# Optimization experiments

Measured on AMD Instinct MI355X. Metric: run time of the kernel, lower is better.

The kernel has to match this reference:

```python
import jax, jax.numpy as jnp
import numpy as np

HID, OUT, EMB, NL = 256, 128, 1024, 4
NR, NP_, NM = 16384, 40000, 30000
E = 200000
NTYPES = 3  # lin_nodes keys: protein, molecule, reaction


def setup_inputs() -> dict:
    key = jax.random.key(0)
    ks = jax.random.split(key, 32)
    f32 = jnp.float32
    inp = {}
    inp["x_reaction"] = jax.random.normal(ks[0], (NR, EMB), f32)
    inp["x_protein"] = jax.random.normal(ks[1], (NP_, EMB), f32)
    inp["x_molecule"] = jax.random.normal(ks[2], (NM, EMB), f32)
    inp["ei_p2r_src"] = jax.random.randint(ks[3], (E,), 0, NP_, jnp.int32)
    inp["ei_p2r_dst"] = jax.random.randint(ks[4], (E,), 0, NR, jnp.int32)
    inp["ei_m2r_src"] = jax.random.randint(ks[5], (E,), 0, NM, jnp.int32)
    inp["ei_m2r_dst"] = jax.random.randint(ks[6], (E,), 0, NR, jnp.int32)
    inp["ei_r2p_src"] = jax.random.randint(ks[7], (E,), 0, NR, jnp.int32)
    inp["ei_r2p_dst"] = jax.random.randint(ks[8], (E,), 0, NP_, jnp.int32)
    inp["ei_r2m_src"] = jax.random.randint(ks[9], (E,), 0, NR, jnp.int32)
    inp["ei_r2m_dst"] = jax.random.randint(ks[10], (E,), 0, NM, jnp.int32)
    inp["output_notes_opt"] = jax.random.normal(ks[11], (NR, EMB), f32)
    inp["output_types"] = jax.random.randint(ks[12], (NR,), 0, NTYPES, jnp.int32)
    s = 0.02
    # layer 0 SAGE params (lazy in_dim = EMB), one set per edge type (4 edge types)
    inp["Wl0"] = jax.random.normal(ks[13], (4, EMB, HID), f32) * s
    inp["Wr0"] = jax.random.normal(ks[14], (4, EMB, HID), f32) * s
    inp["bl0"] = jnp.zeros((4, HID), f32)
    # layers 1..3 SAGE params (in_dim = HID)
    inp["Wl"] = jax.random.normal(ks[15], (NL - 1, 4, HID, HID), f32) * s
    inp["Wr"] = jax.random.normal(ks[16], (NL - 1, 4, HID, HID), f32) * s
    inp["bl"] = jnp.zeros((NL - 1, 4, HID), f32)
    inp["W_reaction"] = jax.random.normal(ks[17], (HID, OUT), f32) * s
    inp["b_reaction"] = jnp.zeros((OUT,), f32)
    inp["W_nodes"] = jax.random.normal(ks[18], (NTYPES, EMB, OUT), f32) * s
    inp["b_nodes"] = jnp.zeros((NTYPES, OUT), f32)
    return inp


def _sage(x_src, x_dst, src, dst, n_dst, Wl, bl, Wr):
    # PyG SAGEConv (aggr='mean'): lin_l(mean_{j->i} x_j) + lin_r(x_i); lin_l has bias.
    g = x_src[src]                                              # [E, d] gather
    s = jax.ops.segment_sum(g, dst, num_segments=n_dst)          # [n_dst, d]
    cnt = jax.ops.segment_sum(jnp.ones((src.shape[0],), x_src.dtype), dst, num_segments=n_dst)
    mean = s / jnp.maximum(cnt, 1.0)[:, None]
    return mean @ Wl + bl + x_dst @ Wr


def _hetero_layer(xr, xp, xm, edges, Wl, bl, Wr):
    # HeteroConv(aggr='sum'): sum SAGE outputs per destination node type.
    (ps, pd), (ms, md), (rps, rpd), (rms, rmd) = edges
    new_r = (_sage(xp, xr, ps, pd, NR, Wl[0], bl[0], Wr[0])
             + _sage(xm, xr, ms, md, NR, Wl[1], bl[1], Wr[1]))
    new_p = _sage(xr, xp, rps, rpd, NP_, Wl[2], bl[2], Wr[2])
    new_m = _sage(xr, xm, rms, rmd, NM, Wl[3], bl[3], Wr[3])
    return new_r, new_p, new_m


def reference(x_reaction, x_protein, x_molecule,
              ei_p2r_src, ei_p2r_dst, ei_m2r_src, ei_m2r_dst,
              ei_r2p_src, ei_r2p_dst, ei_r2m_src, ei_r2m_dst,
              output_notes_opt, output_types,
              Wl0, bl0, Wr0, Wl, bl, Wr,
              W_reaction, b_reaction, W_nodes, b_nodes):
    edges = ((ei_p2r_src, ei_p2r_dst), (ei_m2r_src, ei_m2r_dst),
             (ei_r2p_src, ei_r2p_dst), (ei_r2m_src, ei_r2m_dst))
    xr, xp, xm = _hetero_layer(x_reaction, x_protein, x_molecule, edges, Wl0, bl0, Wr0)
    for l in range(NL - 1):
        xr, xp, xm = _hetero_layer(xr, xp, xm, edges, Wl[l], bl[l], Wr[l])
    reaction_out = xr @ W_reaction + b_reaction                  # [NR, OUT]
    # lin_nodes[t](v) per output node: project with all type linears, select by type id
    projs = jnp.einsum('ke,ted->ktd', output_notes_opt, W_nodes) + b_nodes[None]  # [NR, T, OUT]
    node_out = jnp.take_along_axis(projs, output_types[:, None, None].astype(jnp.int32), axis=1)[:, 0, :]
    # cosine similarity along dim=1, torch-style eps clamp on the norm product
    num = jnp.sum(reaction_out * node_out, axis=-1)
    den = jnp.maximum(jnp.linalg.norm(reaction_out, axis=-1) * jnp.linalg.norm(node_out, axis=-1), 1e-8)
    return (num / den + 1.0) * 0.5
```

## Files before the change

kernel.cpp:

```cpp
#include <hip/hip_runtime.h>
#include <hip/hip_bf16.h>
#include <math.h>
#include <stdint.h>

#define NR_ 16384
#define NP2_ 40000
#define NM_ 30000
#define NE_ 200000
#define EMB_ 1024
#define HID_ 256
#define OUTD_ 128

typedef __attribute__((ext_vector_type(8))) short bf16x8;
typedef __attribute__((ext_vector_type(4))) float f32x4;
typedef __attribute__((ext_vector_type(8))) unsigned short us8;

__device__ __forceinline__ unsigned short f2bf(float f) {
    return __builtin_bit_cast(unsigned short, __float2bfloat16(f));
}
__device__ __forceinline__ float bf2f(unsigned short u) {
    uint32_t v = ((uint32_t)u) << 16;
    return __builtin_bit_cast(float, v);
}

struct Csr4 {
    const int* src[4]; const int* dst[4];
    int* offs[4]; int* cur[4]; int* csr[4];
    int n[4];
};
__global__ void k_zero4(Csr4 c) {
    int y = blockIdx.y;
    int i = blockIdx.x * 256 + threadIdx.x;
    if (i < c.n[y]) c.cur[y][i] = 0;
}
__global__ void k_deg4(Csr4 c) {
    int y = blockIdx.y;
    int i = blockIdx.x * 256 + threadIdx.x;
    if (i < NE_) atomicAdd(&c.cur[y][c.dst[y][i]], 1);
}
__global__ void k_scanA(Csr4 c, int* __restrict__ csum) {
    int y = blockIdx.y;
    int n = c.n[y];
    int ch = blockIdx.x;
    int nch = (n + 1023) >> 10;
    if (ch >= nch) return;
    const int* deg = c.cur[y];
    int* offs = c.offs[y];
    __shared__ int ts[256];
    int base = ch << 10;
    int t = threadIdx.x;
    int v[4];
    int s = 0;
    #pragma unroll
    for (int k = 0; k < 4; ++k) {
        int i = base + t * 4 + k;
        v[k] = (i < n) ? deg[i] : 0;
        s += v[k];
    }
    ts[t] = s;
    __syncthreads();
    for (int st = 1; st < 256; st <<= 1) {
        int x = ts[t];
        int xo = (t >= st) ? ts[t - st] : 0;
        __syncthreads();
        ts[t] = x + xo;
        __syncthreads();
    }
    int run = (t > 0) ? ts[t - 1] : 0;
    #pragma unroll
    for (int k = 0; k < 4; ++k) {
        int i = base + t * 4 + k;
        if (i < n) offs[i] = run;
        run += v[k];
    }
    if (t == 255) csum[y * 40 + ch] = ts[255];
}
__global__ void k_scanB(Csr4 c, int* __restrict__ csum) {
    int y = threadIdx.x;
    if (y < 4) {
        int n = c.n[y];
        int nch = (n + 1023) >> 10;
        int acc = 0;
        for (int i = 0; i < nch; ++i) {
            int v = csum[y * 40 + i];
            csum[y * 40 + i] = acc;
            acc += v;
        }
        c.offs[y][n] = acc;
    }
}
__global__ void k_scanC(Csr4 c, const int* __restrict__ csum) {
    int y = blockIdx.y;
    int i = blockIdx.x * 256 + threadIdx.x;
    if (i < c.n[y]) {
        int v = c.offs[y][i] + csum[y * 40 + (i >> 10)];
        c.offs[y][i] = v;
        c.cur[y][i] = v;
    }
}
__global__ void k_scatter4(Csr4 c) {
    int y = blockIdx.y;
    int i = blockIdx.x * 256 + threadIdx.x;
    if (i < NE_) {
        int d = c.dst[y][i];
        int p = atomicAdd(&c.cur[y][d], 1);
        c.csr[y][p] = c.src[y][i];
    }
}

struct WItem { const float* a; const float* b; unsigned short* dst; int k; int n; };
struct WBatch { WItem it[32]; };
__global__ void k_wconvT(WBatch wb) {
    WItem w = wb.it[blockIdx.y];
    int total = w.k * w.n;
    int kmask = w.k - 1;
    int shift = (w.k == 1024) ? 10 : 8;
    for (int idx = blockIdx.x * 256 + threadIdx.x; idx < total; idx += gridDim.x * 256) {
        int k = idx & kmask, n = idx >> shift;
        float v = w.a[(size_t)k * w.n + n];
        if (w.b) v += w.b[(size_t)k * w.n + n];
        w.dst[idx] = f2bf(v);
    }
}

struct GSeg {
    const void* A; const unsigned short* Bt; void* C; const float* bias;
    int lda, ldc, M, K, ntn, blk0;
};
struct GBatch { GSeg s[3]; int b1, b2, tot; };

template <bool OBF>
__global__ __launch_bounds__(256, 3) void k_gemmb(GBatch gb) {
    __shared__ __align__(16) unsigned short As[128 * 64];
    __shared__ __align__(16) unsigned short Bs[128 * 64];
    const int tid = threadIdx.x;
    const int lane = tid & 63;
    int nwg = gb.tot;
    int o = blockIdx.x;
    int q = nwg >> 3, r = nwg & 7;
    int xcd = o & 7, j = o >> 3;
    int wg = (xcd < r ? xcd * (q + 1) : r * (q + 1) + (xcd - r) * q) + j;
    const int si = (wg >= gb.b1) + (wg >= gb.b2);
    const GSeg sg = gb.s[si];
    const int local = wg - sg.blk0;
    const int bm = (local / sg.ntn) * 128;
    const int bn = (local % sg.ntn) * 128;
    const int lda = sg.lda, ldc = sg.ldc, M = sg.M, K = sg.K;
    const unsigned short* __restrict__ Bt = sg.Bt;
    const float* __restrict__ bias = sg.bias;

    const int wave = tid >> 6;
    const int wr = (wave >> 1) * 64;
    const int wc = (wave & 1) * 64;
    const int frow = lane & 15;
    const int fkc = lane >> 4;
    f32x4 acc[4][4] = {};

    for (int k0 = 0; k0 < K; k0 += 64) {
        #pragma unroll
        for (int i = 0; i < 4; ++i) {
            int c = tid + i * 256;
            int row = c >> 3, kc = c & 7;
            int srck = k0 + ((kc ^ (row & 7)) << 3);
            int ga = min(bm + row, M - 1);
            __builtin_amdgcn_global_load_lds(
                (const __attribute__((address_space(1))) unsigned int*)((const unsigned short*)sg.A + (size_t)ga * lda + srck),
                (__attribute__((address_space(3))) unsigned int*)(As + (size_t)c * 8), 16, 0, 0);
            __builtin_amdgcn_global_load_lds(
                (const __attribute__((address_space(1))) unsigned int*)(Bt + (size_t)(bn + row) * K + srck),
                (__attribute__((address_space(3))) unsigned int*)(Bs + (size_t)c * 8), 16, 0, 0);
        }
        __syncthreads();
        #pragma unroll
        for (int kk = 0; kk < 2; ++kk) {
            bf16x8 af[4], bfr[4];
            #pragma unroll
            for (int m = 0; m < 4; ++m) {
                int row = wr + m * 16 + frow;
                int kc = kk * 4 + fkc;
                af[m] = *(const bf16x8*)(As + (size_t)((row << 3) + (kc ^ (row & 7))) * 8);
            }
            #pragma unroll
            for (int n = 0; n < 4; ++n) {
                int row = wc + n * 16 + frow;
                int kc = kk * 4 + fkc;
                bfr[n] = *(const bf16x8*)(Bs + (size_t)((row << 3) + (kc ^ (row & 7))) * 8);
            }
            #pragma unroll
            for (int m = 0; m < 4; ++m)
                #pragma unroll
                for (int n = 0; n < 4; ++n)
                    acc[m][n] = __builtin_amdgcn_mfma_f32_16x16x32_bf16(bfr[n], af[m], acc[m][n], 0, 0, 0);
        }
        __syncthreads();
    }

    const int ccol0 = (lane >> 4) << 2;
    #pragma unroll
    for (int m = 0; m < 4; ++m) {
        int row = bm + wr + m * 16 + frow;
        if (row < M) {
            #pragma unroll
            for (int n = 0; n < 4; ++n) {
                int col = bn + wc + n * 16 + ccol0;
                f32x4 v = acc[m][n];
                if (bias) {
                    v[0] += bias[col + 0];
                    v[1] += bias[col + 1];
                    v[2] += bias[col + 2];
                    v[3] += bias[col + 3];
                }
                if constexpr (OBF) {
                    ushort4 oo;
                    oo.x = f2bf(v[0]); oo.y = f2bf(v[1]); oo.z = f2bf(v[2]); oo.w = f2bf(v[3]);
                    *(ushort4*)((unsigned short*)sg.C + (size_t)row * ldc + col) = oo;
                } else {
                    *(float4*)((float*)sg.C + (size_t)row * ldc + col) = make_float4(v[0], v[1], v[2], v[3]);
                }
            }
        }
    }
}

template <bool OBF>
__global__ __launch_bounds__(256, 3) void k_gemma(GBatch gb) {
    __shared__ __align__(16) unsigned short As[128 * 64];
    __shared__ __align__(16) unsigned short Bs[2][128 * 64];
    const int tid = threadIdx.x;
    const int lane = tid & 63;
    int nwg = gb.tot;
    int o = blockIdx.x;
    int q = nwg >> 3, r = nwg & 7;
    int xcd = o & 7, j = o >> 3;
    int wg = (xcd < r ? xcd * (q + 1) : r * (q + 1) + (xcd - r) * q) + j;
    const int si = (wg >= gb.b1) + (wg >= gb.b2);
    const GSeg sg = gb.s[si];
    const int local = wg - sg.blk0;
    const int bm = (local / sg.ntn) * 128;
    const int bn = (local % sg.ntn) * 128;
    const int lda = sg.lda, ldc = sg.ldc, M = sg.M, K = sg.K;
    const unsigned short* __restrict__ Bt = sg.Bt;
    const float* __restrict__ bias = sg.bias;

    const int wave = tid >> 6;
    const int wr = (wave >> 1) * 64;
    const int wc = (wave & 1) * 64;
    const int frow = lane & 15;
    const int fkc = lane >> 4;
    f32x4 acc[4][4] = {};
    float4 ra0[4], ra1[4];

#define ALOAD(kk0) do {                                                                    \
    _Pragma("unroll")                                                                      \
    for (int i = 0; i < 4; ++i) {                                                          \
        int c = tid + i * 256, rw = c >> 3, kc = c & 7;                                    \
        int srck = (kk0) + ((kc ^ (rw & 7)) << 3);                                         \
        int ga = min(bm + rw, M - 1);                                                      \
        const float* Af = (const float*)sg.A + (size_t)ga * lda + srck;                    \
        ra0[i] = *(const float4*)Af;                                                       \
        ra1[i] = *(const float4*)(Af + 4);                                                 \
    } } while (0)

#define AWRITE() do {                                                                      \
    _Pragma("unroll")                                                                      \
    for (int i = 0; i < 4; ++i) {                                                          \
        int c = tid + i * 256;                                                             \
        us8 oo;                                                                            \
        oo[0] = f2bf(ra0[i].x); oo[1] = f2bf(ra0[i].y);                                    \
        oo[2] = f2bf(ra0[i].z); oo[3] = f2bf(ra0[i].w);                                    \
        oo[4] = f2bf(ra1[i].x); oo[5] = f2bf(ra1[i].y);                                    \
        oo[6] = f2bf(ra1[i].z); oo[7] = f2bf(ra1[i].w);                                    \
        *(us8*)(As + (size_t)c * 8) = oo;                                                  \
    } } while (0)

#define STAGE_B(bufi, kk0) do {                                                            \
    _Pragma("unroll")                                                                      \
    for (int i = 0; i < 4; ++i) {                                                          \
        int c = tid + i * 256, rw = c >> 3, kc = c & 7;                                    \
        int srck = (kk0) + ((kc ^ (rw & 7)) << 3);                                         \
        __builtin_amdgcn_global_load_lds(                                                  \
            (const __attribute__((address_space(1))) unsigned int*)(Bt + (size_t)(bn + rw) * K + srck), \
            (__attribute__((address_space(3))) unsigned int*)(&Bs[bufi][(size_t)c * 8]), 16, 0, 0); \
    } } while (0)

#define COMPUTE(bufi) do {                                                                 \
    _Pragma("unroll")                                                                      \
    for (int kk = 0; kk < 2; ++kk) {                                                       \
        bf16x8 af[4], bfr[4];                                                              \
        _Pragma("unroll")                                                                  \
        for (int m = 0; m < 4; ++m) {                                                      \
            int rw = wr + m * 16 + frow;                                                   \
            int kc = kk * 4 + fkc;                                                         \
            af[m] = *(const bf16x8*)(As + (size_t)((rw << 3) + (kc ^ (rw & 7))) * 8);      \
        }                                                                                  \
        _Pragma("unroll")                                                                  \
        for (int n = 0; n < 4; ++n) {                                                      \
            int rw = wc + n * 16 + frow;                                                   \
            int kc = kk * 4 + fkc;                                                         \
            bfr[n] = *(const bf16x8*)(&Bs[bufi][(size_t)((rw << 3) + (kc ^ (rw & 7))) * 8]); \
        }                                                                                  \
        _Pragma("unroll")                                                                  \
        for (int m = 0; m < 4; ++m)                                                        \
            _Pragma("unroll")                                                              \
            for (int n = 0; n < 4; ++n)                                                    \
                acc[m][n] = __builtin_amdgcn_mfma_f32_16x16x32_bf16(bfr[n], af[m], acc[m][n], 0, 0, 0); \
    } } while (0)

    const int nt = K >> 6;
    ALOAD(0);
    STAGE_B(0, 0);
    AWRITE();
    asm volatile("s_waitcnt lgkmcnt(0)" ::: "memory");
    __builtin_amdgcn_sched_barrier(0);
    for (int t = 0; t < nt; ++t) {
        if (t + 1 < nt) {
            ALOAD((t + 1) << 6);
            STAGE_B((t + 1) & 1, (t + 1) << 6);
            asm volatile("s_waitcnt vmcnt(12)" ::: "memory");
        } else {
            asm volatile("s_waitcnt vmcnt(0)" ::: "memory");
        }
        __builtin_amdgcn_s_barrier();
        __builtin_amdgcn_sched_barrier(0);
        COMPUTE(t & 1);
        asm volatile("s_waitcnt lgkmcnt(0)" ::: "memory");
        __builtin_amdgcn_s_barrier();
        __builtin_amdgcn_sched_barrier(0);
        if (t + 1 < nt) {
            AWRITE();
            asm volatile("s_waitcnt lgkmcnt(0)" ::: "memory");
            __builtin_amdgcn_sched_barrier(0);
        }
    }
#undef ALOAD
#undef AWRITE
#undef STAGE_B
#undef COMPUTE

    const int ccol0 = (lane >> 4) << 2;
    #pragma unroll
    for (int m = 0; m < 4; ++m) {
        int row = bm + wr + m * 16 + frow;
        if (row < M) {
            #pragma unroll
            for (int n = 0; n < 4; ++n) {
                int col = bn + wc + n * 16 + ccol0;
                f32x4 v = acc[m][n];
                if (bias) {
                    v[0] += bias[col + 0];
                    v[1] += bias[col + 1];
                    v[2] += bias[col + 2];
                    v[3] += bias[col + 3];
                }
                if constexpr (OBF) {
                    ushort4 oo;
                    oo.x = f2bf(v[0]); oo.y = f2bf(v[1]); oo.z = f2bf(v[2]); oo.w = f2bf(v[3]);
                    *(ushort4*)((unsigned short*)sg.C + (size_t)row * ldc + col) = oo;
                } else {
                    *(float4*)((float*)sg.C + (size_t)row * ldc + col) = make_float4(v[0], v[1], v[2], v[3]);
                }
            }
        }
    }
}

struct ASeg {
    const int* offsA; const int* csrA; const unsigned short* projA; int ldpA; const float* biasA;
    const int* offsB; const int* csrB; const unsigned short* projB; int ldpB; const float* biasB;
    unsigned short* outx; int ldo; int ndst; int blk0;
};
struct ABatch { ASeg s[3]; int b1, b2; };

__device__ __forceinline__ void agg_sum16(const int* __restrict__ csr, int beg, int end,
                                          const unsigned short* __restrict__ base, int ldp,
                                          int lane, float* __restrict__ s) {
    int half = lane >> 5;
    for (int b = beg; b < end; b += 64) {
        int cnt = min(64, end - b);
        int myidx = csr[min(b + lane, end - 1)];
        int g = 0;
        for (; g + 3 < cnt; g += 4) {
            int i0 = __shfl(myidx, g + half);
            int i1 = __shfl(myidx, g + 2 + half);
            us8 u0 = *(const us8*)(base + (size_t)i0 * ldp);
            us8 u1 = *(const us8*)(base + (size_t)i1 * ldp);
            #pragma unroll
            for (int j = 0; j < 8; ++j) s[j] += bf2f(u0[j]) + bf2f(u1[j]);
        }
        for (; g + 1 < cnt; g += 2) {
            int i0 = __shfl(myidx, g + half);
            us8 u0 = *(const us8*)(base + (size_t)i0 * ldp);
            #pragma unroll
            for (int j = 0; j < 8; ++j) s[j] += bf2f(u0[j]);
        }
        if (g < cnt) {
            int i0 = __shfl(myidx, g);
            if (half == 0) {
                us8 u0 = *(const us8*)(base + (size_t)i0 * ldp);
                #pragma unroll
                for (int j = 0; j < 8; ++j) s[j] += bf2f(u0[j]);
            }
        }
    }
}

__global__ __launch_bounds__(256) void k_aggb(ABatch ab) {
    int b = blockIdx.x;
    int si = (b >= ab.b1) + (b >= ab.b2);
    const ASeg sg = ab.s[si];
    int node = (b - sg.blk0) * 4 + (threadIdx.x >> 6);
    int lane = threadIdx.x & 63;
    if (node >= sg.ndst) return;
    const int off = (lane & 31) * 8;

    float r[8];
    {
        float s[8] = {};
        int beg = sg.offsA[node], end = sg.offsA[node + 1];
        agg_sum16(sg.csrA, beg, end, sg.projA + off, sg.ldpA, lane, s);
        #pragma unroll
        for (int j = 0; j < 8; ++j) s[j] += __shfl_xor(s[j], 32);
        float inv = 1.f / fmaxf((float)(end - beg), 1.f);
        float4 b0 = *(const float4*)(sg.biasA + off);
        float4 b1 = *(const float4*)(sg.biasA + off + 4);
        r[0] = s[0] * inv + b0.x; r[1] = s[1] * inv + b0.y;
        r[2] = s[2] * inv + b0.z; r[3] = s[3] * inv + b0.w;
        r[4] = s[4] * inv + b1.x; r[5] = s[5] * inv + b1.y;
        r[6] = s[6] * inv + b1.z; r[7] = s[7] * inv + b1.w;
    }
    if (sg.csrB) {
        float s[8] = {};
        int beg = sg.offsB[node], end = sg.offsB[node + 1];
        agg_sum16(sg.csrB, beg, end, sg.projB + off, sg.ldpB, lane, s);
        #pragma unroll
        for (int j = 0; j < 8; ++j) s[j] += __shfl_xor(s[j], 32);
        float inv = 1.f / fmaxf((float)(end - beg), 1.f);
        float4 b0 = *(const float4*)(sg.biasB + off);
        float4 b1 = *(const float4*)(sg.biasB + off + 4);
        r[0] += s[0] * inv + b0.x; r[1] += s[1] * inv + b0.y;
        r[2] += s[2] * inv + b0.z; r[3] += s[3] * inv + b0.w;
        r[4] += s[4] * inv + b1.x; r[5] += s[5] * inv + b1.y;
        r[6] += s[6] * inv + b1.z; r[7] += s[7] * inv + b1.w;
    }

    if (lane < 32) {
        unsigned short* op = sg.outx + (size_t)node * sg.ldo + off;
        us8 cur = *(const us8*)op;
        us8 w;
        #pragma unroll
        for (int j = 0; j < 8; ++j) w[j] = f2bf(bf2f(cur[j]) + r[j]);
        *(us8*)op = w;
    }
}

__global__ __launch_bounds__(256) void k_cos(const float* __restrict__ ro,
                                             const float* __restrict__ pr,
                                             const int* __restrict__ types,
                                             float* __restrict__ out, int nr) {
    int row = blockIdx.x * 4 + (threadIdx.x >> 6);
    int lane = threadIdx.x & 63;
    if (row >= nr) return;
    int t = types[row];
    float2 r = ((const float2*)(ro + (size_t)row * OUTD_))[lane];
    float2 nn = ((const float2*)(pr + (size_t)row * 384 + t * OUTD_))[lane];
    float num = r.x * nn.x + r.y * nn.y;
    float d1 = r.x * r.x + r.y * r.y;
    float d2 = nn.x * nn.x + nn.y * nn.y;
    #pragma unroll
    for (int s = 1; s < 64; s <<= 1) {
        num += __shfl_xor(num, s);
        d1 += __shfl_xor(d1, s);
        d2 += __shfl_xor(d2, s);
    }
    if (lane == 0) out[row] = (num / fmaxf(sqrtf(d1) * sqrtf(d2), 1e-8f) + 1.f) * 0.5f;
}

extern "C" void kernel_launch(void* const* d_in, const int* in_sizes, int n_in,
                              void* d_out, int out_size, void* d_ws, size_t ws_size,
                              hipStream_t stream) {
    const float* x_r0 = (const float*)d_in[0];
    const float* x_p0 = (const float*)d_in[1];
    const float* x_m0 = (const float*)d_in[2];
    const int* e_src[4] = {(const int*)d_in[3], (const int*)d_in[5], (const int*)d_in[7], (const int*)d_in[9]};
    const int* e_dst[4] = {(const int*)d_in[4], (const int*)d_in[6], (const int*)d_in[8], (const int*)d_in[10]};
    const float* notes = (const float*)d_in[11];
    const int* types = (const int*)d_in[12];
    const float* Wl0 = (const float*)d_in[13];
    const float* Wr0 = (const float*)d_in[14];
    const float* bl0 = (const float*)d_in[15];
    const float* WlL = (const float*)d_in[16];
    const float* WrL = (const float*)d_in[17];
    const float* blL = (const float*)d_in[18];
    const float* Wre = (const float*)d_in[19];
    const float* bre = (const float*)d_in[20];
    const float* Wn  = (const float*)d_in[21];
    const float* bn  = (const float*)d_in[22];
    float* out = (float*)d_out;

    uintptr_t base = (uintptr_t)d_ws;
    auto alloc = [&](size_t bytes) -> void* {
        uintptr_t p = (base + 255) & ~(uintptr_t)255;
        base = p + bytes;
        return (void*)p;
    };
    unsigned short* Rb[2] = {(unsigned short*)alloc((size_t)NR_ * 768 * 2),
                             (unsigned short*)alloc((size_t)NR_ * 768 * 2)};
    unsigned short* Pb[2] = {(unsigned short*)alloc((size_t)NP2_ * 512 * 2),
                             (unsigned short*)alloc((size_t)NP2_ * 512 * 2)};
    unsigned short* Mb[2] = {(unsigned short*)alloc((size_t)NM_ * 512 * 2),
                             (unsigned short*)alloc((size_t)NM_ * 512 * 2)};
    float* ro = (float*)alloc((size_t)NR_ * OUTD_ * 4);
    float* pr = (float*)alloc((size_t)NR_ * 384 * 4);
    unsigned short* wbf = (unsigned short*)alloc((size_t)4000000 * 2);
    int* csum = (int*)alloc(160 * 4);
    int nd[4] = {NR_, NR_, NP2_, NM_};
    Csr4 cs{};
    for (int t = 0; t < 4; ++t) {
        cs.src[t] = e_src[t]; cs.dst[t] = e_dst[t]; cs.n[t] = nd[t];
        cs.offs[t] = (int*)alloc(((size_t)nd[t] + 1) * 4);
        cs.cur[t]  = (int*)alloc((size_t)nd[t] * 4);
        cs.csr[t]  = (int*)alloc((size_t)NE_ * 4);
    }

    unsigned short *BR[4], *BP[4], *BM[4], *Bre, *Bn;
    {
        WBatch wb{};
        int cnt = 0;
        size_t woff = 0;
        auto add = [&](const float* a, const float* bb, int K, int N) -> unsigned short* {
            unsigned short* dst = wbf + woff;
            woff += (size_t)K * N;
            wb.it[cnt] = WItem{a, bb, dst, K, N};
            ++cnt;
            return dst;
        };
        const size_t w0 = (size_t)EMB_ * HID_;
        const size_t wl = (size_t)HID_ * HID_;
        for (int l = 0; l < 4; ++l) {
            int K = (l == 0) ? EMB_ : HID_;
            const float* Wr_ = (l == 0) ? Wr0 : WrL + (size_t)(l - 1) * 4 * wl;
            const float* Wl_ = (l == 0) ? Wl0 : WlL + (size_t)(l - 1) * 4 * wl;
            size_t ws_ = (l == 0) ? w0 : wl;
            BR[l] = add(Wr_ + 0 * ws_, Wr_ + 1 * ws_, K, HID_);
            add(Wl_ + 2 * ws_, nullptr, K, HID_);
            add(Wl_ + 3 * ws_, nullptr, K, HID_);
            BP[l] = add(Wr_ + 2 * ws_, nullptr, K, HID_);
            add(Wl_ + 0 * ws_, nullptr, K, HID_);
            BM[l] = add(Wr_ + 3 * ws_, nullptr, K, HID_);
            add(Wl_ + 1 * ws_, nullptr, K, HID_);
        }
        Bre = add(Wre, nullptr, HID_, OUTD_);
        Bn = add(Wn + 0 * (size_t)EMB_ * OUTD_, nullptr, EMB_, OUTD_);
        add(Wn + 1 * (size_t)EMB_ * OUTD_, nullptr, EMB_, OUTD_);
        add(Wn + 2 * (size_t)EMB_ * OUTD_, nullptr, EMB_, OUTD_);
        k_wconvT<<<dim3(128, cnt), 256, 0, stream>>>(wb);
    }

    k_zero4<<<dim3((NP2_ + 255) / 256, 4), 256, 0, stream>>>(cs);
    k_deg4<<<dim3((NE_ + 255) / 256, 4), 256, 0, stream>>>(cs);
    k_scanA<<<dim3(40, 4), 256, 0, stream>>>(cs, csum);
    k_scanB<<<1, 64, 0, stream>>>(cs, csum);
    k_scanC<<<dim3((NP2_ + 255) / 256, 4), 256, 0, stream>>>(cs, csum);
    k_scatter4<<<dim3((NE_ + 255) / 256, 4), 256, 0, stream>>>(cs);

    const int MT_R = (NR_ + 127) / 128;
    const int MT_P = (NP2_ + 127) / 128;
    const int MT_M = (NM_ + 127) / 128;
    auto seg = [](const void* A, const unsigned short* Bt, void* C, const float* bias,
                  int lda, int ldc, int M, int K, int ntn, int blk0) -> GSeg {
        return GSeg{A, Bt, C, bias, lda, ldc, M, K, ntn, blk0};
    };

    const int AB_R = (NR_ + 3) / 4, AB_P = (NP2_ + 3) / 4, AB_M = (NM_ + 3) / 4;

    for (int l = 0; l < 4; ++l) {
        int K = (l == 0) ? EMB_ : HID_;
        unsigned short* R = Rb[l & 1];
        unsigned short* P = Pb[l & 1];
        unsigned short* M = Mb[l & 1];
        const float* bl_ = (l == 0) ? bl0 : blL + (size_t)(l - 1) * 4 * HID_;

        GBatch gb{};
        int nR = MT_R * 6, nP = MT_P * 4, nM = MT_M * 4;
        if (l == 0) {
            gb.s[0] = seg(x_r0, BR[0], R, nullptr, EMB_, 768, NR_, EMB_, 6, 0);
            gb.s[1] = seg(x_p0, BP[0], P, nullptr, EMB_, 512, NP2_, EMB_, 4, nR);
            gb.s[2] = seg(x_m0, BM[0], M, nullptr, EMB_, 512, NM_, EMB_, 4, nR + nP);
        } else {
            gb.s[0] = seg(Rb[(l - 1) & 1], BR[l], R, nullptr, 768, 768, NR_, K, 6, 0);
            gb.s[1] = seg(Pb[(l - 1) & 1], BP[l], P, nullptr, 512, 512, NP2_, K, 4, nR);
            gb.s[2] = seg(Mb[(l - 1) & 1], BM[l], M, nullptr, 512, 512, NM_, K, 4, nR + nP);
        }
        gb.b1 = nR; gb.b2 = nR + nP; gb.tot = nR + nP + nM;
        if (l == 0) k_gemma<true><<<gb.tot, 256, 0, stream>>>(gb);
        else        k_gemmb<true><<<gb.tot, 256, 0, stream>>>(gb);

        ABatch ab{};
        ab.s[0] = ASeg{cs.offs[0], cs.csr[0], P + 256, 512, bl_ + 0 * HID_,
                       cs.offs[1], cs.csr[1], M + 256, 512, bl_ + 1 * HID_,
                       R, 768, NR_, 0};
        ab.s[1] = ASeg{cs.offs[2], cs.csr[2], R + 256, 768, bl_ + 2 * HID_,
                       nullptr, nullptr, nullptr, 0, nullptr,
                       P, 512, NP2_, AB_R};
        ab.s[2] = ASeg{cs.offs[3], cs.csr[3], R + 512, 768, bl_ + 3 * HID_,
                       nullptr, nullptr, nullptr, 0, nullptr,
                       M, 512, NM_, AB_R + AB_P};
        ab.b1 = AB_R; ab.b2 = AB_R + AB_P;
        k_aggb<<<AB_R + AB_P + AB_M, 256, 0, stream>>>(ab);
    }

    {
        GBatch g1{};
        g1.s[0] = seg(Rb[1], Bre, ro, bre, 768, OUTD_, NR_, HID_, 1, 0);
        g1.b1 = g1.b2 = g1.tot = MT_R;
        k_gemmb<false><<<g1.tot, 256, 0, stream>>>(g1);
        GBatch g2{};
        g2.s[0] = seg(notes, Bn, pr, bn, EMB_, 384, NR_, EMB_, 3, 0);
        g2.b1 = g2.b2 = g2.tot = MT_R * 3;
        k_gemma<false><<<g2.tot, 256, 0, stream>>>(g2);
    }
    k_cos<<<NR_ / 4, 256, 0, stream>>>(ro, pr, types, out, NR_);
}
```

Before: 746.0 us.

## Group output rows by type and project each only with its own node linear

Rows of output_notes_opt are bucketed by type id through a histogram, a padded base offset per type and a scatter. A new gathered GEMM then projects each 128-row tile with only its type's weight matrix, instead of computing all three projections and selecting one. This drops about two thirds of the node-projection FLOPs and the A-matrix reads. The cost is four small preprocessing kernels, a gathered A load with indirect row access, and padding rows that point at row 0.

```diff
diff --git a/kernel.cpp b/kernel.cpp
--- a/kernel.cpp
+++ b/kernel.cpp
@@ -105,6 +105,35 @@
         int d = c.dst[y][i];
         int p = atomicAdd(&c.cur[y][d], 1);
         c.csr[y][p] = c.src[y][i];
+    }
+}
+
+#define PERM_CAP (131 * 128)
+__global__ void k_tzero(int* meta, int* perm) {
+    int i = blockIdx.x * 256 + threadIdx.x;
+    if (i < 8) meta[i] = 0;
+    if (i < PERM_CAP) perm[i] = 0;
+}
+__global__ void k_thist(const int* __restrict__ types, int* __restrict__ meta) {
+    int i = blockIdx.x * 256 + threadIdx.x;
+    if (i < NR_) atomicAdd(&meta[types[i]], 1);
+}
+__global__ void k_tbase(int* meta) {
+    if (threadIdx.x == 0) {
+        meta[8] = 0;
+        meta[9]  = meta[8] + ((meta[0] + 127) & ~127);
+        meta[10] = meta[9] + ((meta[1] + 127) & ~127);
+        meta[11] = meta[10] + ((meta[2] + 127) & ~127);
+    }
+}
+__global__ void k_tscatter(const int* __restrict__ types, int* __restrict__ meta,
+                           int* __restrict__ perm, int* __restrict__ inv) {
+    int i = blockIdx.x * 256 + threadIdx.x;
+    if (i < NR_) {
+        int t = types[i];
+        int pos = meta[8 + t] + atomicAdd(&meta[4 + t], 1);
+        perm[pos] = i;
+        inv[i] = pos;
     }
 }
 
@@ -332,10 +361,6 @@
             __builtin_amdgcn_sched_barrier(0);
         }
     }
-#undef ALOAD
-#undef AWRITE
-#undef STAGE_B
-#undef COMPUTE
 
     const int ccol0 = (lane >> 4) << 2;
     #pragma unroll
@@ -362,6 +387,140 @@
             }
         }
     }
+#undef ALOAD
+#undef AWRITE
+#undef STAGE_B
+#undef COMPUTE
+}
+
+__global__ __launch_bounds__(256, 3) void k_gemmp(const float* __restrict__ A,
+                                                  const unsigned short* __restrict__ Bt3,
+                                                  const float* __restrict__ bias3,
+                                                  float* __restrict__ C,
+                                                  const int* __restrict__ perm,
+                                                  const int* __restrict__ meta) {
+    int t1 = meta[9] >> 7, t2 = meta[10] >> 7, t3 = meta[11] >> 7;
+    int tb = blockIdx.x;
+    if (tb >= t3) return;
+    const int si = (tb >= t1) + (tb >= t2);
+    const unsigned short* __restrict__ Bt = Bt3 + (size_t)si * EMB_ * OUTD_;
+    const float* __restrict__ bias = bias3 + si * OUTD_;
+    const int bm = tb * 128;
+    const int tid = threadIdx.x;
+    const int lane = tid & 63;
+    const int wave = tid >> 6;
+    const int wr = (wave >> 1) * 64;
+    const int wc = (wave & 1) * 64;
+    const int frow = lane & 15;
+    const int fkc = lane >> 4;
+
+    __shared__ __align__(16) unsigned short As[128 * 64];
+    __shared__ __align__(16) unsigned short Bs[2][128 * 64];
+    f32x4 acc[4][4] = {};
+    float4 ra0[4], ra1[4];
+
+#define ALOAD(kk0) do {                                                                    \
+    _Pragma("unroll")                                                                      \
+    for (int i = 0; i < 4; ++i) {                                                          \
+        int c = tid + i * 256, rw = c >> 3, kc = c & 7;                                    \
+        int srck = (kk0) + ((kc ^ (rw & 7)) << 3);                                         \
+        int ga = perm[bm + rw];                                                            \
+        const float* Af = A + (size_t)ga * EMB_ + srck;                                    \
+        ra0[i] = *(const float4*)Af;                                                       \
+        ra1[i] = *(const float4*)(Af + 4);                                                 \
+    } } while (0)
+
+#define AWRITE() do {                                                                      \
+    _Pragma("unroll")                                                                      \
+    for (int i = 0; i < 4; ++i) {                                                          \
+        int c = tid + i * 256;                                                             \
+        us8 oo;                                                                            \
+        oo[0] = f2bf(ra0[i].x); oo[1] = f2bf(ra0[i].y);                                    \
+        oo[2] = f2bf(ra0[i].z); oo[3] = f2bf(ra0[i].w);                                    \
+        oo[4] = f2bf(ra1[i].x); oo[5] = f2bf(ra1[i].y);                                    \
+        oo[6] = f2bf(ra1[i].z); oo[7] = f2bf(ra1[i].w);                                    \
+        *(us8*)(As + (size_t)c * 8) = oo;                                                  \
+    } } while (0)
+
+#define STAGE_B(bufi, kk0) do {                                                            \
+    _Pragma("unroll")                                                                      \
+    for (int i = 0; i < 4; ++i) {                                                          \
+        int c = tid + i * 256, rw = c >> 3, kc = c & 7;                                    \
+        int srck = (kk0) + ((kc ^ (rw & 7)) << 3);                                         \
+        __builtin_amdgcn_global_load_lds(                                                  \
+            (const __attribute__((address_space(1))) unsigned int*)(Bt + (size_t)rw * EMB_ + srck), \
+            (__attribute__((address_space(3))) unsigned int*)(&Bs[bufi][(size_t)c * 8]), 16, 0, 0); \
+    } } while (0)
+
+#define COMPUTE(bufi) do {                                                                 \
+    _Pragma("unroll")                                                                      \
+    for (int kk = 0; kk < 2; ++kk) {                                                       \
+        bf16x8 af[4], bfr[4];                                                              \
+        _Pragma("unroll")                                                                  \
+        for (int m = 0; m < 4; ++m) {                                                      \
+            int rw = wr + m * 16 + frow;                                                   \
+            int kc = kk * 4 + fkc;                                                         \
+            af[m] = *(const bf16x8*)(As + (size_t)((rw << 3) + (kc ^ (rw & 7))) * 8);      \
+        }                                                                                  \
+        _Pragma("unroll")                                                                  \
+        for (int n = 0; n < 4; ++n) {                                                      \
+            int rw = wc + n * 16 + frow;                                                   \
+            int kc = kk * 4 + fkc;                                                         \
+            bfr[n] = *(const bf16x8*)(&Bs[bufi][(size_t)((rw << 3) + (kc ^ (rw & 7))) * 8]); \
+        }                                                                                  \
+        _Pragma("unroll")                                                                  \
+        for (int m = 0; m < 4; ++m)                                                        \
+            _Pragma("unroll")                                                              \
+            for (int n = 0; n < 4; ++n)                                                    \
+                acc[m][n] = __builtin_amdgcn_mfma_f32_16x16x32_bf16(bfr[n], af[m], acc[m][n], 0, 0, 0); \
+    } } while (0)
+
+    const int nt = EMB_ >> 6;
+    ALOAD(0);
+    STAGE_B(0, 0);
+    AWRITE();
+    asm volatile("s_waitcnt lgkmcnt(0)" ::: "memory");
+    __builtin_amdgcn_sched_barrier(0);
+    for (int t = 0; t < nt; ++t) {
+        if (t + 1 < nt) {
+            ALOAD((t + 1) << 6);
+            STAGE_B((t + 1) & 1, (t + 1) << 6);
+            asm volatile("s_waitcnt vmcnt(12)" ::: "memory");
+        } else {
+            asm volatile("s_waitcnt vmcnt(0)" ::: "memory");
+        }
+        __builtin_amdgcn_s_barrier();
+        __builtin_amdgcn_sched_barrier(0);
+        COMPUTE(t & 1);
+        asm volatile("s_waitcnt lgkmcnt(0)" ::: "memory");
+        __builtin_amdgcn_s_barrier();
+        __builtin_amdgcn_sched_barrier(0);
+        if (t + 1 < nt) {
+            AWRITE();
+            asm volatile("s_waitcnt lgkmcnt(0)" ::: "memory");
+            __builtin_amdgcn_sched_barrier(0);
+        }
+    }
+#undef ALOAD
+#undef AWRITE
+#undef STAGE_B
+#undef COMPUTE
+
+    const int ccol0 = (lane >> 4) << 2;
+    #pragma unroll
+    for (int m = 0; m < 4; ++m) {
+        int row = bm + wr + m * 16 + frow;
+        #pragma unroll
+        for (int n = 0; n < 4; ++n) {
+            int col = wc + n * 16 + ccol0;
+            f32x4 v = acc[m][n];
+            v[0] += bias[col + 0];
+            v[1] += bias[col + 1];
+            v[2] += bias[col + 2];
+            v[3] += bias[col + 3];
+            *(float4*)(C + (size_t)row * OUTD_ + col) = make_float4(v[0], v[1], v[2], v[3]);
+        }
+    }
 }
 
 struct ASeg {
@@ -455,14 +614,14 @@
 
 __global__ __launch_bounds__(256) void k_cos(const float* __restrict__ ro,
                                              const float* __restrict__ pr,
-                                             const int* __restrict__ types,
+                                             const int* __restrict__ inv,
                                              float* __restrict__ out, int nr) {
     int row = blockIdx.x * 4 + (threadIdx.x >> 6);
     int lane = threadIdx.x & 63;
     if (row >= nr) return;
-    int t = types[row];
+    int pos = inv[row];
     float2 r = ((const float2*)(ro + (size_t)row * OUTD_))[lane];
-    float2 nn = ((const float2*)(pr + (size_t)row * 384 + t * OUTD_))[lane];
+    float2 nn = ((const float2*)(pr + (size_t)pos * OUTD_))[lane];
     float num = r.x * nn.x + r.y * nn.y;
     float d1 = r.x * r.x + r.y * r.y;
     float d2 = nn.x * nn.x + nn.y * nn.y;
@@ -510,9 +669,12 @@
     unsigned short* Mb[2] = {(unsigned short*)alloc((size_t)NM_ * 512 * 2),
                              (unsigned short*)alloc((size_t)NM_ * 512 * 2)};
     float* ro = (float*)alloc((size_t)NR_ * OUTD_ * 4);
-    float* pr = (float*)alloc((size_t)NR_ * 384 * 4);
+    float* pr = (float*)alloc((size_t)PERM_CAP * OUTD_ * 4);
     unsigned short* wbf = (unsigned short*)alloc((size_t)4000000 * 2);
     int* csum = (int*)alloc(160 * 4);
+    int* meta = (int*)alloc(16 * 4);
+    int* perm = (int*)alloc(PERM_CAP * 4);
+    int* inv  = (int*)alloc(NR_ * 4);
     int nd[4] = {NR_, NR_, NP2_, NM_};
     Csr4 cs{};
     for (int t = 0; t < 4; ++t) {
@@ -556,6 +718,11 @@
         k_wconvT<<<dim3(128, cnt), 256, 0, stream>>>(wb);
     }
 
+    k_tzero<<<(PERM_CAP + 255) / 256, 256, 0, stream>>>(meta, perm);
+    k_thist<<<(NR_ + 255) / 256, 256, 0, stream>>>(types, meta);
+    k_tbase<<<1, 64, 0, stream>>>(meta);
+    k_tscatter<<<(NR_ + 255) / 256, 256, 0, stream>>>(types, meta, perm, inv);
+
     k_zero4<<<dim3((NP2_ + 255) / 256, 4), 256, 0, stream>>>(cs);
     k_deg4<<<dim3((NE_ + 255) / 256, 4), 256, 0, stream>>>(cs);
     k_scanA<<<dim3(40, 4), 256, 0, stream>>>(cs, csum);
@@ -614,10 +781,7 @@
         g1.s[0] = seg(Rb[1], Bre, ro, bre, 768, OUTD_, NR_, HID_, 1, 0);
         g1.b1 = g1.b2 = g1.tot = MT_R;
         k_gemmb<false><<<g1.tot, 256, 0, stream>>>(g1);
-        GBatch g2{};
-        g2.s[0] = seg(notes, Bn, pr, bn, EMB_, 384, NR_, EMB_, 3, 0);
-        g2.b1 = g2.b2 = g2.tot = MT_R * 3;
-        k_gemma<false><<<g2.tot, 256, 0, stream>>>(g2);
-    }
-    k_cos<<<NR_ / 4, 256, 0, stream>>>(ro, pr, types, out, NR_);
-}
+        k_gemmp<<<PERM_CAP / 128, 256, 0, stream>>>(notes, Bn, bn, pr, perm, meta);
+    }
+    k_cos<<<NR_ / 4, 256, 0, stream>>>(ro, pr, inv, out, NR_);
+}
```

Measured after the change: 973.9 us. +30.6%, slower.
